# Performance work log

Hardware: AMD Instinct MI355X
Metric: run time of the kernel (lower is better)

Reference implementation:

```python
import jax, jax.numpy as jnp
import numpy as np

N_NODES = 10000
N_EDGES = 640000
F_IN = 128
HID = 128
N_LAYERS = 3
N_ACT = 4096
NEG_SLOPE = 0.2


def setup_inputs() -> dict:
    key = jax.random.key(0)
    ks = jax.random.split(key, 16)
    s = 0.05
    return {
        "x": jax.random.normal(ks[0], (N_NODES, F_IN), jnp.float32),
        "edge_index": jax.random.randint(ks[1], (2, N_EDGES), 0, N_NODES, jnp.int64),
        "action_src": jax.random.randint(ks[2], (N_ACT,), 0, N_NODES, jnp.int64),
        "action_dst": jax.random.randint(ks[3], (N_ACT,), 0, N_NODES, jnp.int64),
        "action_type": jax.random.randint(ks[4], (N_ACT,), 0, 2, jnp.int32),
        "gat_W": jax.random.normal(ks[5], (N_LAYERS, HID, HID), jnp.float32) * s,
        "gat_asrc": jax.random.normal(ks[6], (N_LAYERS, HID), jnp.float32) * s,
        "gat_adst": jax.random.normal(ks[7], (N_LAYERS, HID), jnp.float32) * s,
        "gat_b": jax.random.normal(ks[8], (N_LAYERS, HID), jnp.float32) * s,
        "mlp_W1": jax.random.normal(ks[9], (2 * HID + 1, HID), jnp.float32) * s,
        "mlp_b1": jax.random.normal(ks[10], (HID,), jnp.float32) * s,
        "mlp_W2": jax.random.normal(ks[11], (HID, 1), jnp.float32) * s,
        "mlp_b2": jax.random.normal(ks[12], (1,), jnp.float32) * s,
    }


def _gat_layer(h, src, dst, W, a_src, a_dst, b, n_nodes):
    # PyG GATConv, heads=1: z = h W; e_ij = leaky_relu(a_src.z_j + a_dst.z_i)
    z = h @ W                                   # [N, HID]
    e = jax.nn.leaky_relu((z @ a_src)[src] + (z @ a_dst)[dst], NEG_SLOPE)  # [E+N]
    m = jax.ops.segment_max(e, dst, num_segments=n_nodes)
    m = jnp.where(jnp.isfinite(m), m, 0.0)
    ex = jnp.exp(e - m[dst])
    denom = jax.ops.segment_sum(ex, dst, num_segments=n_nodes)
    alpha = ex / denom[dst]                     # softmax over incoming edges
    out = jax.ops.segment_sum(alpha[:, None] * z[src], dst, num_segments=n_nodes)
    return out + b


def reference(x, edge_index, action_src, action_dst, action_type,
              gat_W, gat_asrc, gat_adst, gat_b,
              mlp_W1, mlp_b1, mlp_W2, mlp_b2):
    n = x.shape[0]
    loop = jnp.arange(n, dtype=edge_index.dtype)  # add_self_loops=True
    src = jnp.concatenate([edge_index[0], loop])
    dst = jnp.concatenate([edge_index[1], loop])
    h = x
    for l in range(N_LAYERS):
        h = jax.nn.relu(_gat_layer(h, src, dst, gat_W[l], gat_asrc[l], gat_adst[l], gat_b[l], n))
    # vectorized action scoring: [h[src], h[dst], type_flag] -> MLP -> scalar
    feat = jnp.concatenate(
        [h[action_src], h[action_dst], action_type.astype(h.dtype)[:, None]], axis=-1)
    hidden = jax.nn.relu(feat @ mlp_W1 + mlp_b1)
    scores = (hidden @ mlp_W2 + mlp_b2)[:, 0]   # [N_ACT]
    return scores
```

## Files before the change

### kernel.cpp

```cpp
#include <hip/hip_runtime.h>
#include <hip/hip_bf16.h>
#include <hip/hip_fp16.h>

#define N_NODES 10000
#define N_EDGES 640000
#define TOT_E   (N_EDGES + N_NODES)
#define HID     128
#define NEG_SLOPE 0.2f
#define N_ACT   4096

#define NBKT   250
#define NPB    40
#define P1_EPB 4096
#define P1_EPT 16
#define P1_BLOCKS 159
#define SLOTP  56

__global__ __launch_bounds__(256) void part1_k(const int* __restrict__ ei,
                                               unsigned* __restrict__ bpart,
                                               int* __restrict__ bcnt) {
    __shared__ int hist[256];
    __shared__ int lofs[256];
    __shared__ int sc[256];
    __shared__ unsigned stage[P1_EPB];
    __shared__ unsigned char bkt_of[P1_EPB];
    int t = threadIdx.x;
    hist[t] = 0;
    __syncthreads();

    unsigned pk[P1_EPT];
    int bk[P1_EPT];
    int e0 = blockIdx.x * P1_EPB;
#pragma unroll
    for (int i = 0; i < P1_EPT; i++) {
        int e = e0 + i * 256 + t;
        if (e < TOT_E) {
            int src, dst;
            if (e < N_EDGES) { src = ei[e]; dst = ei[N_EDGES + e]; }
            else             { src = e - N_EDGES; dst = src; }
            pk[i] = ((unsigned)dst << 16) | (unsigned)src;
            bk[i] = dst / NPB;
            atomicAdd(&hist[bk[i]], 1);
        } else bk[i] = -1;
    }
    __syncthreads();
    int v = hist[t];
    sc[t] = v;
    __syncthreads();
    for (int o = 1; o < 256; o <<= 1) {
        int u = (t >= o) ? sc[t - o] : 0;
        __syncthreads();
        sc[t] += u;
        __syncthreads();
    }
    lofs[t] = sc[t] - v;
    bcnt[blockIdx.x * 256 + t] = v;
    hist[t] = 0;
    __syncthreads();
#pragma unroll
    for (int i = 0; i < P1_EPT; i++) {
        if (bk[i] >= 0) {
            int p = atomicAdd(&hist[bk[i]], 1);
            int slot = lofs[bk[i]] + p;
            stage[slot] = pk[i];
            bkt_of[slot] = (unsigned char)bk[i];
        }
    }
    __syncthreads();
    int nv = min(P1_EPB, TOT_E - e0);
    for (int s = t; s < nv; s += 256) {
        int b = bkt_of[s];
        bpart[b * (P1_BLOCKS * SLOTP) + blockIdx.x * SLOTP + (s - lofs[b])] = stage[s];
    }
}

__global__ __launch_bounds__(256) void part2_k(const unsigned* __restrict__ bpart,
                                               const int* __restrict__ bcnt,
                                               int* __restrict__ csr,
                                               int* __restrict__ offs) {
    __shared__ unsigned ebuf[4096];
    __shared__ int sc[256];
    __shared__ int nhist[NPB];
    __shared__ int bstart_s, cnt_s;
    int b = blockIdx.x, t = threadIdx.x;

    int tot = 0;
    if (t < NBKT)
        for (int blk = 0; blk < P1_BLOCKS; blk++) tot += bcnt[blk * 256 + t];
    sc[t] = (t < NBKT) ? tot : 0;
    __syncthreads();
    for (int o = 1; o < 256; o <<= 1) {
        int u = (t >= o) ? sc[t - o] : 0;
        __syncthreads();
        sc[t] += u;
        __syncthreads();
    }
    if (t == b) { bstart_s = sc[t] - tot; cnt_s = tot; }
    if (b == 0 && t == 255) offs[N_NODES] = sc[255];
    __syncthreads();

    int L = (t < P1_BLOCKS) ? bcnt[t * 256 + b] : 0;
    sc[t] = L;
    __syncthreads();
    for (int o = 1; o < 256; o <<= 1) {
        int u = (t >= o) ? sc[t - o] : 0;
        __syncthreads();
        sc[t] += u;
        __syncthreads();
    }
    int P = sc[t] - L;
    if (t < NPB) nhist[t] = 0;
    if (t < P1_BLOCKS && L > 0) {
        const unsigned* myrun = bpart + b * (P1_BLOCKS * SLOTP) + t * SLOTP;
        for (int i = 0; i < L; i++) ebuf[P + i] = myrun[i];
    }
    __syncthreads();

    int cnt = cnt_s;
    int n0 = b * NPB;
    for (int i = t; i < cnt; i += 256) atomicAdd(&nhist[(ebuf[i] >> 16) - n0], 1);
    __syncthreads();
    if (t < 64) {
        int v2 = (t < NPB) ? nhist[t] : 0;
        int s2 = v2;
        for (int o = 1; o < 64; o <<= 1) {
            int u = __shfl_up(s2, o, 64);
            if (t >= o) s2 += u;
        }
        if (t < NPB) {
            int ofs = bstart_s + s2 - v2;
            nhist[t] = ofs;
            offs[n0 + t] = ofs;
        }
    }
    __syncthreads();
    for (int i = t; i < cnt; i += 256) {
        unsigned pk = ebuf[i];
        int p = atomicAdd(&nhist[(pk >> 16) - n0], 1);
        csr[p] = pk & 0xFFFF;
    }
}

__device__ __forceinline__ void agg_node(const __half2* __restrict__ z2,
                                         const float* __restrict__ zsi, float zdn,
                                         const int* __restrict__ csr, int o0, int deg,
                                         int lane, float& accx, float& accy, float& denom) {
    for (int base = 0; base < deg; base += 64) {
        int j = base + lane;
        int sreg = 0;
        float ex = 0.f;
        if (j < deg) {
            int s = csr[o0 + j];
            sreg = s;
            float e = zsi[s] + zdn;
            e = e > 0.f ? e : NEG_SLOPE * e;
            ex = __expf(e);
        }
        int cnt = min(64, deg - base);
        int q = 0;
        for (; q + 8 <= cnt; q += 8) {
#pragma unroll
            for (int u = 0; u < 8; u++) {
                int sq = __builtin_amdgcn_readlane(sreg, q + u);
                float exq = __uint_as_float(
                    __builtin_amdgcn_readlane(__float_as_uint(ex), q + u));
                denom += exq;
                float2 vf = __half22float2(z2[sq * 64]);
                accx = fmaf(exq, vf.x, accx);
                accy = fmaf(exq, vf.y, accy);
            }
        }
        for (; q < cnt; q++) {
            int sq = __builtin_amdgcn_readlane(sreg, q);
            float exq = __uint_as_float(
                __builtin_amdgcn_readlane(__float_as_uint(ex), q));
            denom += exq;
            float2 vf = __half22float2(z2[sq * 64]);
            accx = fmaf(exq, vf.x, accx);
            accy = fmaf(exq, vf.y, accy);
        }
    }
}


__global__ __launch_bounds__(256, 4) void gemm_k(const float* __restrict__ A,
                                                 const float* __restrict__ W,
                                                 const float* __restrict__ avs,
                                                 const float* __restrict__ avd,
                                                 __half* __restrict__ z16,
                                                 float* __restrict__ zs,
                                                 float* __restrict__ zd) {
    __shared__ float Wc[2][32 * HID];
    int t = threadIdx.x;
    float4 wreg[4];
    {
        const float4* Wg = (const float4*)W;
#pragma unroll
        for (int i = 0; i < 4; i++) wreg[i] = Wg[t + 256 * i];
    }
    int tx = t & 31;
    int ty = t >> 5;
    int row0 = blockIdx.x * 16 + ty * 2;
    float acc[2][4] = {{0.f}};
    float4 a_nxt[2];
#pragma unroll
    for (int r = 0; r < 2; r++) a_nxt[r] = *(const float4*)&A[(row0 + r) * HID];

    for (int c = 0; c < 4; c++) {
        float4* dstb = (float4*)Wc[c & 1];
#pragma unroll
        for (int i = 0; i < 4; i++) dstb[t + 256 * i] = wreg[i];
        __syncthreads();
        if (c + 1 < 4) {
            const float4* Wg = (const float4*)(W + (c + 1) * 32 * HID);
#pragma unroll
            for (int i = 0; i < 4; i++) wreg[i] = Wg[t + 256 * i];
        }
        const float* Wb = Wc[c & 1];
#pragma unroll
        for (int k8 = 0; k8 < 32; k8 += 4) {
            float a_cur[2][4];
#pragma unroll
            for (int r = 0; r < 2; r++) {
                a_cur[r][0] = a_nxt[r].x; a_cur[r][1] = a_nxt[r].y;
                a_cur[r][2] = a_nxt[r].z; a_cur[r][3] = a_nxt[r].w;
            }
            int kn = c * 32 + k8 + 4;
            if (kn < HID) {
#pragma unroll
                for (int r = 0; r < 2; r++)
                    a_nxt[r] = *(const float4*)&A[(row0 + r) * HID + kn];
            }
#pragma unroll
            for (int kk = 0; kk < 4; kk++) {
                float4 wv = *(const float4*)&Wb[(k8 + kk) * HID + tx * 4];
#pragma unroll
                for (int r = 0; r < 2; r++) {
                    acc[r][0] = fmaf(a_cur[r][kk], wv.x, acc[r][0]);
                    acc[r][1] = fmaf(a_cur[r][kk], wv.y, acc[r][1]);
                    acc[r][2] = fmaf(a_cur[r][kk], wv.z, acc[r][2]);
                    acc[r][3] = fmaf(a_cur[r][kk], wv.w, acc[r][3]);
                }
            }
        }
    }
    float4 asv = *(const float4*)&avs[tx * 4];
    float4 adv = *(const float4*)&avd[tx * 4];
#pragma unroll
    for (int r = 0; r < 2; r++) {
        int row = row0 + r;
        *(__half2*)&z16[row * HID + tx * 4]     = __floats2half2_rn(acc[r][0], acc[r][1]);
        *(__half2*)&z16[row * HID + tx * 4 + 2] = __floats2half2_rn(acc[r][2], acc[r][3]);
        float ps = acc[r][0] * asv.x + acc[r][1] * asv.y + acc[r][2] * asv.z + acc[r][3] * asv.w;
        float pd = acc[r][0] * adv.x + acc[r][1] * adv.y + acc[r][2] * adv.z + acc[r][3] * adv.w;
#pragma unroll
        for (int o = 1; o < 32; o <<= 1) {
            ps += __shfl_xor(ps, o, 64);
            pd += __shfl_xor(pd, o, 64);
        }
        if (tx == 0) { zs[row] = ps; zd[row] = pd; }
    }
}


__global__ __launch_bounds__(256, 4) void fuse_k(const __half* __restrict__ z16i,
                                                 const float* __restrict__ zsi,
                                                 const float* __restrict__ zdi,
                                                 const int* __restrict__ offs,
                                                 const int* __restrict__ csr,
                                                 const float* __restrict__ bprev,
                                                 const float* __restrict__ W,
                                                 const float* __restrict__ avs,
                                                 const float* __restrict__ avd,
                                                 __half* __restrict__ z16o,
                                                 float* __restrict__ zso,
                                                 float* __restrict__ zdo) {
    __shared__ float hT[8][HID];
    __shared__ float Wc[2][32 * HID];
    int t = threadIdx.x;
    int w = t >> 6, lane = t & 63;
    int n0 = blockIdx.x * 8;
    float4 wreg[4];
    {
        const float4* Wg = (const float4*)W;
#pragma unroll
        for (int i = 0; i < 4; i++) wreg[i] = Wg[t + 256 * i];
    }
    const __half2* z2 = (const __half2*)z16i + lane;

    float2 bv = *(const float2*)&bprev[2 * lane];
#pragma unroll
    for (int i = 0; i < 2; i++) {
        int ln = w * 2 + i;
        int n = n0 + ln;
        int o0 = offs[n];
        int deg = offs[n + 1] - o0;
        float zdn = zdi[n];
        float accx = 0.f, accy = 0.f, denom = 0.f;
        agg_node(z2, zsi, zdn, csr, o0, deg, lane, accx, accy, denom);
        float inv = 1.0f / denom;
        float vx = accx * inv + bv.x;
        float vy = accy * inv + bv.y;
        float2 hv;
        hv.x = vx > 0.f ? vx : 0.f;
        hv.y = vy > 0.f ? vy : 0.f;
        *(float2*)&hT[ln][2 * lane] = hv;
    }

    int tx = t & 31, ty = t >> 5;
    float acc[4] = {0.f, 0.f, 0.f, 0.f};
    for (int c = 0; c < 4; c++) {
        float4* dstb = (float4*)Wc[c & 1];
#pragma unroll
        for (int i = 0; i < 4; i++) dstb[t + 256 * i] = wreg[i];
        __syncthreads();
        if (c + 1 < 4) {
            const float4* Wg = (const float4*)(W + (c + 1) * 32 * HID);
#pragma unroll
            for (int i = 0; i < 4; i++) wreg[i] = Wg[t + 256 * i];
        }
        const float* Wb = Wc[c & 1];
        const float* h0 = &hT[ty][c * 32];
#pragma unroll 8
        for (int kk = 0; kk < 32; kk++) {
            float f0 = h0[kk];
            float4 wv = *(const float4*)&Wb[kk * HID + tx * 4];
            acc[0] = fmaf(f0, wv.x, acc[0]);
            acc[1] = fmaf(f0, wv.y, acc[1]);
            acc[2] = fmaf(f0, wv.z, acc[2]);
            acc[3] = fmaf(f0, wv.w, acc[3]);
        }
    }
    float4 asv = *(const float4*)&avs[tx * 4];
    float4 adv = *(const float4*)&avd[tx * 4];
    int row = n0 + ty;
    *(__half2*)&z16o[row * HID + tx * 4]     = __floats2half2_rn(acc[0], acc[1]);
    *(__half2*)&z16o[row * HID + tx * 4 + 2] = __floats2half2_rn(acc[2], acc[3]);
    float ps = acc[0] * asv.x + acc[1] * asv.y + acc[2] * asv.z + acc[3] * asv.w;
    float pd = acc[0] * adv.x + acc[1] * adv.y + acc[2] * adv.z + acc[3] * adv.w;
#pragma unroll
    for (int o = 1; o < 32; o <<= 1) {
        ps += __shfl_xor(ps, o, 64);
        pd += __shfl_xor(pd, o, 64);
    }
    if (tx == 0) { zso[row] = ps; zdo[row] = pd; }
}


__global__ __launch_bounds__(256) void agg_k(const __half* __restrict__ z16,
                                             const float* __restrict__ zs,
                                             const float* __restrict__ zd,
                                             const int* __restrict__ offs,
                                             const int* __restrict__ csr,
                                             const float* __restrict__ b,
                                             float* __restrict__ hout) {
    int t = threadIdx.x;
    int w = t >> 6, lane = t & 63;
    int n = blockIdx.x * 4 + w;
    if (n >= N_NODES) return;
    int o0 = offs[n];
    int deg = offs[n + 1] - o0;
    float zdn = zd[n];
    const __half2* z2 = (const __half2*)z16 + lane;
    float accx = 0.f, accy = 0.f, denom = 0.f;
    agg_node(z2, zs, zdn, csr, o0, deg, lane, accx, accy, denom);
    float inv = 1.0f / denom;
    float2 bv = *(const float2*)&b[2 * lane];
    float vx = accx * inv + bv.x;
    float vy = accy * inv + bv.y;
    float2 o;
    o.x = vx > 0.f ? vx : 0.f;
    o.y = vy > 0.f ? vy : 0.f;
    *(float2*)&hout[n * HID + 2 * lane] = o;
}


#define SC_APB 16

__global__ __launch_bounds__(256) void score_k(const float* __restrict__ h,
                                               const int* __restrict__ asrc,
                                               const int* __restrict__ adst,
                                               const int* __restrict__ atype,
                                               const float* __restrict__ W1,
                                               const float* __restrict__ b1,
                                               const float* __restrict__ W2,
                                               const float* __restrict__ b2,
                                               float* __restrict__ out) {
    __shared__ float featT[257][SC_APB + 1];
    __shared__ float Wc[2][32 * HID];
    int t = threadIdx.x;
    int a0 = blockIdx.x * SC_APB;

    float4 wreg[4];
    {
        const float4* Wg = (const float4*)W1;
#pragma unroll
        for (int i = 0; i < 4; i++) wreg[i] = Wg[t + 256 * i];
    }
    for (int idx = t; idx < SC_APB * 128; idx += 256) {
        int a = idx >> 7, c = idx & 127;
        featT[c][a]       = h[asrc[a0 + a] * HID + c];
        featT[128 + c][a] = h[adst[a0 + a] * HID + c];
    }
    if (t < SC_APB) featT[256][t] = (float)atype[a0 + t];

    int cg = t & 31, ap = t >> 5;
    float4 bv = *(const float4*)&b1[cg * 4];
    float acc0[4] = {bv.x, bv.y, bv.z, bv.w};
    float acc1[4] = {bv.x, bv.y, bv.z, bv.w};

    for (int c = 0; c < 8; c++) {
        float4* dstb = (float4*)Wc[c & 1];
#pragma unroll
        for (int i = 0; i < 4; i++) dstb[t + 256 * i] = wreg[i];
        __syncthreads();
        if (c + 1 < 8) {
            const float4* Wg = (const float4*)(W1 + (c + 1) * 32 * HID);
#pragma unroll
            for (int i = 0; i < 4; i++) wreg[i] = Wg[t + 256 * i];
        }
        const float* Wb = Wc[c & 1];
        const float* fT = &featT[c * 32][0];
#pragma unroll 8
        for (int kk = 0; kk < 32; kk++) {
            float4 wv = *(const float4*)&Wb[kk * HID + cg * 4];
            float f0 = fT[kk * (SC_APB + 1) + ap * 2];
            float f1 = fT[kk * (SC_APB + 1) + ap * 2 + 1];
            acc0[0] = fmaf(f0, wv.x, acc0[0]);
            acc0[1] = fmaf(f0, wv.y, acc0[1]);
            acc0[2] = fmaf(f0, wv.z, acc0[2]);
            acc0[3] = fmaf(f0, wv.w, acc0[3]);
            acc1[0] = fmaf(f1, wv.x, acc1[0]);
            acc1[1] = fmaf(f1, wv.y, acc1[1]);
            acc1[2] = fmaf(f1, wv.z, acc1[2]);
            acc1[3] = fmaf(f1, wv.w, acc1[3]);
        }
    }
    {
        float4 wv = *(const float4*)&W1[256 * HID + cg * 4];
        float f0 = featT[256][ap * 2];
        float f1 = featT[256][ap * 2 + 1];
        acc0[0] = fmaf(f0, wv.x, acc0[0]); acc0[1] = fmaf(f0, wv.y, acc0[1]);
        acc0[2] = fmaf(f0, wv.z, acc0[2]); acc0[3] = fmaf(f0, wv.w, acc0[3]);
        acc1[0] = fmaf(f1, wv.x, acc1[0]); acc1[1] = fmaf(f1, wv.y, acc1[1]);
        acc1[2] = fmaf(f1, wv.z, acc1[2]); acc1[3] = fmaf(f1, wv.w, acc1[3]);
    }
    float4 w2v = *(const float4*)&W2[cg * 4];
    float v0 = 0.f, v1 = 0.f;
    v0 += (acc0[0] > 0.f ? acc0[0] : 0.f) * w2v.x;
    v0 += (acc0[1] > 0.f ? acc0[1] : 0.f) * w2v.y;
    v0 += (acc0[2] > 0.f ? acc0[2] : 0.f) * w2v.z;
    v0 += (acc0[3] > 0.f ? acc0[3] : 0.f) * w2v.w;
    v1 += (acc1[0] > 0.f ? acc1[0] : 0.f) * w2v.x;
    v1 += (acc1[1] > 0.f ? acc1[1] : 0.f) * w2v.y;
    v1 += (acc1[2] > 0.f ? acc1[2] : 0.f) * w2v.z;
    v1 += (acc1[3] > 0.f ? acc1[3] : 0.f) * w2v.w;
#pragma unroll
    for (int o = 1; o < 32; o <<= 1) {
        v0 += __shfl_xor(v0, o, 64);
        v1 += __shfl_xor(v1, o, 64);
    }
    if (cg == 0) {
        out[a0 + ap * 2]     = v0 + b2[0];
        out[a0 + ap * 2 + 1] = v1 + b2[0];
    }
}


extern "C" void kernel_launch(void* const* d_in, const int* in_sizes, int n_in,
                              void* d_out, int out_size, void* d_ws, size_t ws_size,
                              hipStream_t stream) {
    const float* x   = (const float*)d_in[0];
    const int* ei    = (const int*)d_in[1];
    const int* asrc  = (const int*)d_in[2];
    const int* adst  = (const int*)d_in[3];
    const int* atype = (const int*)d_in[4];
    const float* gW  = (const float*)d_in[5];
    const float* gas = (const float*)d_in[6];
    const float* gad = (const float*)d_in[7];
    const float* gb  = (const float*)d_in[8];
    const float* W1  = (const float*)d_in[9];
    const float* b1  = (const float*)d_in[10];
    const float* W2  = (const float*)d_in[11];
    const float* b2  = (const float*)d_in[12];
    float* out = (float*)d_out;

    __half* z16A = (__half*)d_ws;
    __half* z16B = z16A + N_NODES * HID;
    float* h3   = (float*)(z16B + N_NODES * HID);
    float* zsA  = h3 + N_NODES * HID;
    float* zdA  = zsA + N_NODES;
    float* zsB  = zdA + N_NODES;
    float* zdB  = zsB + N_NODES;
    int* offs   = (int*)(zdB + N_NODES);
    int* csr    = offs + (N_NODES + 1);
    int* bcnt   = csr + TOT_E;
    unsigned* bpart = (unsigned*)(bcnt + P1_BLOCKS * 256);

    part1_k<<<P1_BLOCKS, 256, 0, stream>>>(ei, bpart, bcnt);
    part2_k<<<NBKT, 256, 0, stream>>>(bpart, bcnt, csr, offs);

    gemm_k<<<N_NODES / 16, 256, 0, stream>>>(x, gW, gas, gad, z16A, zsA, zdA);
    fuse_k<<<N_NODES / 8, 256, 0, stream>>>(z16A, zsA, zdA, offs, csr, gb,
                                            gW + 1 * HID * HID, gas + 1 * HID, gad + 1 * HID,
                                            z16B, zsB, zdB);
    fuse_k<<<N_NODES / 8, 256, 0, stream>>>(z16B, zsB, zdB, offs, csr, gb + 1 * HID,
                                            gW + 2 * HID * HID, gas + 2 * HID, gad + 2 * HID,
                                            z16A, zsA, zdA);
    agg_k<<<(N_NODES + 3) / 4, 256, 0, stream>>>(z16A, zsA, zdA, offs, csr,
                                                 gb + 2 * HID, h3);
    score_k<<<N_ACT / SC_APB, 256, 0, stream>>>(h3, asrc, adst, atype,
                                                W1, b1, W2, b2, out);
}
```

Baseline: 249.7 us.

## Merge layer-0 GEMM and edge partition into one heterogeneous kernel launch

Combines the independent first-layer GEMM and the edge bucketing pass (part1) into a single launch, dispatching on block index and sharing LDS through a union. This removes one kernel launch and lets the memory-bound partition overlap with the compute-bound GEMM. It also raises the gather unroll in the aggregation loop from 8 to 16 to put more loads in flight. The union makes LDS per block the size of the larger branch, and the wider unroll adds register pressure.

```diff
diff --git a/kernel.cpp b/kernel.cpp
--- a/kernel.cpp
+++ b/kernel.cpp
@@ -15,62 +15,154 @@
 #define P1_EPT 16
 #define P1_BLOCKS 159
 #define SLOTP  56
-
-__global__ __launch_bounds__(256) void part1_k(const int* __restrict__ ei,
-                                               unsigned* __restrict__ bpart,
-                                               int* __restrict__ bcnt) {
-    __shared__ int hist[256];
-    __shared__ int lofs[256];
-    __shared__ int sc[256];
-    __shared__ unsigned stage[P1_EPB];
-    __shared__ unsigned char bkt_of[P1_EPB];
+#define GEMM_BLOCKS (N_NODES / 16)
+
+
+union ComboLDS {
+    struct {
+        int hist[256];
+        int lofs[256];
+        int sc[256];
+        unsigned stage[P1_EPB];
+        unsigned char bkt_of[P1_EPB];
+    } p1;
+    struct {
+        float Wc[2][32 * HID];
+    } g;
+};
+
+__global__ __launch_bounds__(256, 4) void combo_k(const float* __restrict__ A,
+                                                  const float* __restrict__ W,
+                                                  const float* __restrict__ avs,
+                                                  const float* __restrict__ avd,
+                                                  __half* __restrict__ z16,
+                                                  float* __restrict__ zs,
+                                                  float* __restrict__ zd,
+                                                  const int* __restrict__ ei,
+                                                  unsigned* __restrict__ bpart,
+                                                  int* __restrict__ bcnt) {
+    __shared__ ComboLDS u;
     int t = threadIdx.x;
-    hist[t] = 0;
-    __syncthreads();
-
-    unsigned pk[P1_EPT];
-    int bk[P1_EPT];
-    int e0 = blockIdx.x * P1_EPB;
-#pragma unroll
-    for (int i = 0; i < P1_EPT; i++) {
-        int e = e0 + i * 256 + t;
-        if (e < TOT_E) {
-            int src, dst;
-            if (e < N_EDGES) { src = ei[e]; dst = ei[N_EDGES + e]; }
-            else             { src = e - N_EDGES; dst = src; }
-            pk[i] = ((unsigned)dst << 16) | (unsigned)src;
-            bk[i] = dst / NPB;
-            atomicAdd(&hist[bk[i]], 1);
-        } else bk[i] = -1;
-    }
-    __syncthreads();
-    int v = hist[t];
-    sc[t] = v;
-    __syncthreads();
-    for (int o = 1; o < 256; o <<= 1) {
-        int u = (t >= o) ? sc[t - o] : 0;
-        __syncthreads();
-        sc[t] += u;
-        __syncthreads();
-    }
-    lofs[t] = sc[t] - v;
-    bcnt[blockIdx.x * 256 + t] = v;
-    hist[t] = 0;
-    __syncthreads();
-#pragma unroll
-    for (int i = 0; i < P1_EPT; i++) {
-        if (bk[i] >= 0) {
-            int p = atomicAdd(&hist[bk[i]], 1);
-            int slot = lofs[bk[i]] + p;
-            stage[slot] = pk[i];
-            bkt_of[slot] = (unsigned char)bk[i];
-        }
-    }
-    __syncthreads();
-    int nv = min(P1_EPB, TOT_E - e0);
-    for (int s = t; s < nv; s += 256) {
-        int b = bkt_of[s];
-        bpart[b * (P1_BLOCKS * SLOTP) + blockIdx.x * SLOTP + (s - lofs[b])] = stage[s];
+    int bid = blockIdx.x;
+
+    if (bid < GEMM_BLOCKS) {
+        float4 wreg[4];
+        {
+            const float4* Wg = (const float4*)W;
+#pragma unroll
+            for (int i = 0; i < 4; i++) wreg[i] = Wg[t + 256 * i];
+        }
+        int tx = t & 31;
+        int ty = t >> 5;
+        int row0 = bid * 16 + ty * 2;
+        float acc[2][4] = {{0.f}};
+        float4 a_nxt[2];
+#pragma unroll
+        for (int r = 0; r < 2; r++) a_nxt[r] = *(const float4*)&A[(row0 + r) * HID];
+
+        for (int c = 0; c < 4; c++) {
+            float4* dstb = (float4*)u.g.Wc[c & 1];
+#pragma unroll
+            for (int i = 0; i < 4; i++) dstb[t + 256 * i] = wreg[i];
+            __syncthreads();
+            if (c + 1 < 4) {
+                const float4* Wg = (const float4*)(W + (c + 1) * 32 * HID);
+#pragma unroll
+                for (int i = 0; i < 4; i++) wreg[i] = Wg[t + 256 * i];
+            }
+            const float* Wb = u.g.Wc[c & 1];
+#pragma unroll
+            for (int k8 = 0; k8 < 32; k8 += 4) {
+                float a_cur[2][4];
+#pragma unroll
+                for (int r = 0; r < 2; r++) {
+                    a_cur[r][0] = a_nxt[r].x; a_cur[r][1] = a_nxt[r].y;
+                    a_cur[r][2] = a_nxt[r].z; a_cur[r][3] = a_nxt[r].w;
+                }
+                int kn = c * 32 + k8 + 4;
+                if (kn < HID) {
+#pragma unroll
+                    for (int r = 0; r < 2; r++)
+                        a_nxt[r] = *(const float4*)&A[(row0 + r) * HID + kn];
+                }
+#pragma unroll
+                for (int kk = 0; kk < 4; kk++) {
+                    float4 wv = *(const float4*)&Wb[(k8 + kk) * HID + tx * 4];
+#pragma unroll
+                    for (int r = 0; r < 2; r++) {
+                        acc[r][0] = fmaf(a_cur[r][kk], wv.x, acc[r][0]);
+                        acc[r][1] = fmaf(a_cur[r][kk], wv.y, acc[r][1]);
+                        acc[r][2] = fmaf(a_cur[r][kk], wv.z, acc[r][2]);
+                        acc[r][3] = fmaf(a_cur[r][kk], wv.w, acc[r][3]);
+                    }
+                }
+            }
+        }
+        float4 asv = *(const float4*)&avs[tx * 4];
+        float4 adv = *(const float4*)&avd[tx * 4];
+#pragma unroll
+        for (int r = 0; r < 2; r++) {
+            int row = row0 + r;
+            *(__half2*)&z16[row * HID + tx * 4]     = __floats2half2_rn(acc[r][0], acc[r][1]);
+            *(__half2*)&z16[row * HID + tx * 4 + 2] = __floats2half2_rn(acc[r][2], acc[r][3]);
+            float ps = acc[r][0] * asv.x + acc[r][1] * asv.y + acc[r][2] * asv.z + acc[r][3] * asv.w;
+            float pd = acc[r][0] * adv.x + acc[r][1] * adv.y + acc[r][2] * adv.z + acc[r][3] * adv.w;
+#pragma unroll
+            for (int o = 1; o < 32; o <<= 1) {
+                ps += __shfl_xor(ps, o, 64);
+                pd += __shfl_xor(pd, o, 64);
+            }
+            if (tx == 0) { zs[row] = ps; zd[row] = pd; }
+        }
+    } else {
+        int blk = bid - GEMM_BLOCKS;
+        u.p1.hist[t] = 0;
+        __syncthreads();
+
+        unsigned pk[P1_EPT];
+        int bk[P1_EPT];
+        int e0 = blk * P1_EPB;
+#pragma unroll
+        for (int i = 0; i < P1_EPT; i++) {
+            int e = e0 + i * 256 + t;
+            if (e < TOT_E) {
+                int src, dst;
+                if (e < N_EDGES) { src = ei[e]; dst = ei[N_EDGES + e]; }
+                else             { src = e - N_EDGES; dst = src; }
+                pk[i] = ((unsigned)dst << 16) | (unsigned)src;
+                bk[i] = dst / NPB;
+                atomicAdd(&u.p1.hist[bk[i]], 1);
+            } else bk[i] = -1;
+        }
+        __syncthreads();
+        int v = u.p1.hist[t];
+        u.p1.sc[t] = v;
+        __syncthreads();
+        for (int o = 1; o < 256; o <<= 1) {
+            int uu = (t >= o) ? u.p1.sc[t - o] : 0;
+            __syncthreads();
+            u.p1.sc[t] += uu;
+            __syncthreads();
+        }
+        u.p1.lofs[t] = u.p1.sc[t] - v;
+        bcnt[blk * 256 + t] = v;
+        u.p1.hist[t] = 0;
+        __syncthreads();
+#pragma unroll
+        for (int i = 0; i < P1_EPT; i++) {
+            if (bk[i] >= 0) {
+                int p = atomicAdd(&u.p1.hist[bk[i]], 1);
+                int slot = u.p1.lofs[bk[i]] + p;
+                u.p1.stage[slot] = pk[i];
+                u.p1.bkt_of[slot] = (unsigned char)bk[i];
+            }
+        }
+        __syncthreads();
+        int nv = min(P1_EPB, TOT_E - e0);
+        for (int s = t; s < nv; s += 256) {
+            int b = u.p1.bkt_of[s];
+            bpart[b * (P1_BLOCKS * SLOTP) + blk * SLOTP + (s - u.p1.lofs[b])] = u.p1.stage[s];
+        }
     }
 }
 
@@ -158,9 +250,9 @@
         }
         int cnt = min(64, deg - base);
         int q = 0;
-        for (; q + 8 <= cnt; q += 8) {
-#pragma unroll
-            for (int u = 0; u < 8; u++) {
+        for (; q + 16 <= cnt; q += 16) {
+#pragma unroll
+            for (int u = 0; u < 16; u++) {
                 int sq = __builtin_amdgcn_readlane(sreg, q + u);
                 float exq = __uint_as_float(
                     __builtin_amdgcn_readlane(__float_as_uint(ex), q + u));
@@ -179,86 +271,6 @@
             accx = fmaf(exq, vf.x, accx);
             accy = fmaf(exq, vf.y, accy);
         }
-    }
-}
-
-
-__global__ __launch_bounds__(256, 4) void gemm_k(const float* __restrict__ A,
-                                                 const float* __restrict__ W,
-                                                 const float* __restrict__ avs,
-                                                 const float* __restrict__ avd,
-                                                 __half* __restrict__ z16,
-                                                 float* __restrict__ zs,
-                                                 float* __restrict__ zd) {
-    __shared__ float Wc[2][32 * HID];
-    int t = threadIdx.x;
-    float4 wreg[4];
-    {
-        const float4* Wg = (const float4*)W;
-#pragma unroll
-        for (int i = 0; i < 4; i++) wreg[i] = Wg[t + 256 * i];
-    }
-    int tx = t & 31;
-    int ty = t >> 5;
-    int row0 = blockIdx.x * 16 + ty * 2;
-    float acc[2][4] = {{0.f}};
-    float4 a_nxt[2];
-#pragma unroll
-    for (int r = 0; r < 2; r++) a_nxt[r] = *(const float4*)&A[(row0 + r) * HID];
-
-    for (int c = 0; c < 4; c++) {
-        float4* dstb = (float4*)Wc[c & 1];
-#pragma unroll
-        for (int i = 0; i < 4; i++) dstb[t + 256 * i] = wreg[i];
-        __syncthreads();
-        if (c + 1 < 4) {
-            const float4* Wg = (const float4*)(W + (c + 1) * 32 * HID);
-#pragma unroll
-            for (int i = 0; i < 4; i++) wreg[i] = Wg[t + 256 * i];
-        }
-        const float* Wb = Wc[c & 1];
-#pragma unroll
-        for (int k8 = 0; k8 < 32; k8 += 4) {
-            float a_cur[2][4];
-#pragma unroll
-            for (int r = 0; r < 2; r++) {
-                a_cur[r][0] = a_nxt[r].x; a_cur[r][1] = a_nxt[r].y;
-                a_cur[r][2] = a_nxt[r].z; a_cur[r][3] = a_nxt[r].w;
-            }
-            int kn = c * 32 + k8 + 4;
-            if (kn < HID) {
-#pragma unroll
-                for (int r = 0; r < 2; r++)
-                    a_nxt[r] = *(const float4*)&A[(row0 + r) * HID + kn];
-            }
-#pragma unroll
-            for (int kk = 0; kk < 4; kk++) {
-                float4 wv = *(const float4*)&Wb[(k8 + kk) * HID + tx * 4];
-#pragma unroll
-                for (int r = 0; r < 2; r++) {
-                    acc[r][0] = fmaf(a_cur[r][kk], wv.x, acc[r][0]);
-                    acc[r][1] = fmaf(a_cur[r][kk], wv.y, acc[r][1]);
-                    acc[r][2] = fmaf(a_cur[r][kk], wv.z, acc[r][2]);
-                    acc[r][3] = fmaf(a_cur[r][kk], wv.w, acc[r][3]);
-                }
-            }
-        }
-    }
-    float4 asv = *(const float4*)&avs[tx * 4];
-    float4 adv = *(const float4*)&avd[tx * 4];
-#pragma unroll
-    for (int r = 0; r < 2; r++) {
-        int row = row0 + r;
-        *(__half2*)&z16[row * HID + tx * 4]     = __floats2half2_rn(acc[r][0], acc[r][1]);
-        *(__half2*)&z16[row * HID + tx * 4 + 2] = __floats2half2_rn(acc[r][2], acc[r][3]);
-        float ps = acc[r][0] * asv.x + acc[r][1] * asv.y + acc[r][2] * asv.z + acc[r][3] * asv.w;
-        float pd = acc[r][0] * adv.x + acc[r][1] * adv.y + acc[r][2] * adv.z + acc[r][3] * adv.w;
-#pragma unroll
-        for (int o = 1; o < 32; o <<= 1) {
-            ps += __shfl_xor(ps, o, 64);
-            pd += __shfl_xor(pd, o, 64);
-        }
-        if (tx == 0) { zs[row] = ps; zd[row] = pd; }
     }
 }
 
@@ -497,10 +509,11 @@
     int* bcnt   = csr + TOT_E;
     unsigned* bpart = (unsigned*)(bcnt + P1_BLOCKS * 256);
 
-    part1_k<<<P1_BLOCKS, 256, 0, stream>>>(ei, bpart, bcnt);
+    combo_k<<<GEMM_BLOCKS + P1_BLOCKS, 256, 0, stream>>>(x, gW, gas, gad,
+                                                         z16A, zsA, zdA,
+                                                         ei, bpart, bcnt);
     part2_k<<<NBKT, 256, 0, stream>>>(bpart, bcnt, csr, offs);
 
-    gemm_k<<<N_NODES / 16, 256, 0, stream>>>(x, gW, gas, gad, z16A, zsA, zdA);
     fuse_k<<<N_NODES / 8, 256, 0, stream>>>(z16A, zsA, zdA, offs, csr, gb,
                                             gW + 1 * HID * HID, gas + 1 * HID, gad + 1 * HID,
                                             z16B, zsB, zdB);
```

New measurement: 246.3 us. No clear change (-1.4%).
